# Optimization experiments

Hardware: AMD Instinct MI355X
Metric: run time of the kernel (lower is better)

Reference implementation:

```python
import jax, jax.numpy as jnp
import numpy as np
from jax import lax

CIN, COUT, K, PAD = 256, 128, 3, 1


def setup_inputs() -> dict:
    key = jax.random.key(0)
    ks = jax.random.split(key, 5)
    N, h0, w0 = 2, 64, 64
    x = jax.random.normal(ks[0], (N, CIN, h0, w0), jnp.float32)
    lateral_feat = jax.random.normal(ks[1], (N, COUT, 1, 1), jnp.float32)
    trans_w = jax.random.normal(ks[2], (CIN, COUT, K, K), jnp.float32) * 0.02
    off_w1 = jax.random.normal(ks[3], (64, COUT, 3, 3), jnp.float32) * 0.02
    off_b1 = jnp.zeros((64,), jnp.float32)
    off_w2 = jax.random.normal(ks[4], (2 * K * K, 64, 3, 3), jnp.float32) * 0.02
    off_b2 = jnp.zeros((2 * K * K,), jnp.float32)
    return dict(x=x, lateral_feat=lateral_feat, trans_w=trans_w,
                off_w1=off_w1, off_b1=off_b1, off_w2=off_w2, off_b2=off_b2)


def _conv2d(x, w, b, pad):
    y = lax.conv_general_dilated(x, w, (1, 1), [(pad, pad), (pad, pad)],
                                 dimension_numbers=('NCHW', 'OIHW', 'NCHW'))
    return y + b[None, :, None, None]


def _conv_transpose2d(x, w, stride, pad, out_pad):
    # torch ConvTranspose2d weight layout: [Cin, Cout, k, k]
    k = w.shape[2]
    wt = jnp.flip(w, (2, 3)).transpose(1, 0, 2, 3)  # [Cout, Cin, k, k]
    lo = k - 1 - pad
    hi = k - 1 - pad + out_pad
    return lax.conv_general_dilated(x, wt, (1, 1), [(lo, hi), (lo, hi)],
                                    lhs_dilation=(stride, stride),
                                    dimension_numbers=('NCHW', 'OIHW', 'NCHW'))


def _deform_conv2d(x, offset, w, pad):
    # x [N,C,H,W], offset [N,2*K*K,H,W] (y,x interleaved per kernel tap), w [O,C,K,K]
    N, C, H, W = x.shape
    O = w.shape[0]
    KK = K * K
    off = offset.reshape(N, KK, 2, H, W)
    ky = jnp.arange(KK) // K
    kx = jnp.arange(KK) % K
    py = jnp.arange(H)[None, None, :, None] + (ky - pad)[None, :, None, None] + off[:, :, 0]
    px = jnp.arange(W)[None, None, None, :] + (kx - pad)[None, :, None, None] + off[:, :, 1]
    y0 = jnp.floor(py)
    x0 = jnp.floor(px)
    dy = py - y0
    dx = px - x0
    y0i = y0.astype(jnp.int32)
    x0i = x0.astype(jnp.int32)
    xf = x.reshape(N, C, H * W)

    def corner(yi, xi, wgt):
        valid = (yi >= 0) & (yi < H) & (xi >= 0) & (xi < W)
        idx = (jnp.clip(yi, 0, H - 1) * W + jnp.clip(xi, 0, W - 1)).reshape(N, -1)
        v = jnp.take_along_axis(xf, idx[:, None, :], axis=2).reshape(N, C, KK, H, W)
        return v * (wgt * valid)[:, None]

    sampled = (corner(y0i, x0i, (1 - dy) * (1 - dx))
               + corner(y0i, x0i + 1, (1 - dy) * dx)
               + corner(y0i + 1, x0i, dy * (1 - dx))
               + corner(y0i + 1, x0i + 1, dy * dx))  # [N,C,KK,H,W]
    return jnp.einsum('nckhw,ock->nohw', sampled, w.reshape(O, C, KK))


def reference(x, lateral_feat, trans_w, off_w1, off_b1, off_w2, off_b2):
    up = _conv_transpose2d(x, trans_w, 2, PAD, 1)          # [N, COUT, 2h0, 2w0]
    h = jax.nn.relu(_conv2d(lateral_feat, off_w1, off_b1, 1))
    offset = jnp.tanh(_conv2d(h, off_w2, off_b2, 1))       # [N, 18, 1, 1]
    N, C, H, W = up.shape
    # offset.repeat(1, 1, H, W) with 1x1 spatial input == broadcast to full grid
    offset = jnp.broadcast_to(offset, (N, 2 * K * K, H, W))
    # deform_conv2d uses trans_conv weight [O=CIN, I=COUT, K, K], stride=1, pad=PAD
    return _deform_conv2d(up, offset, trans_w, PAD)        # [N, CIN, H, W]
```

## Files before the change

### kernel.cpp

```cpp
#include <hip/hip_runtime.h>
#include <hip/hip_fp16.h>
#include <math.h>

typedef __attribute__((ext_vector_type(8))) _Float16 f16x8;
typedef __attribute__((ext_vector_type(4))) float f32x4;

__device__ __forceinline__ unsigned short f2h(float f) {
    __half h = __float2half_rn(f);
    union { __half h; unsigned short u; } v; v.h = h; return v.u;
}
__device__ __forceinline__ unsigned pk2h(float lo, float hi) {
    __half2 h = __floats2half2_rn(lo, hi);
    union { __half2 h; unsigned u; } v; v.h = h; return v.u;
}

#define BARRIER() do { asm volatile("s_waitcnt lgkmcnt(0)" ::: "memory"); \
                       __builtin_amdgcn_s_barrier(); } while (0)

__device__ __forceinline__ void blend_store_h(uint4 uA, uint4 uB, uint4 uC, uint4 uD,
                                              __half2 w0, __half2 w1, __half2 w2, __half2 w3,
                                              unsigned short* dst) {
    union U { uint4 u; __half2 h[4]; };
    U a, b, c, d, r;
    a.u = uA; b.u = uB; c.u = uC; d.u = uD;
#pragma unroll
    for (int i = 0; i < 4; ++i)
        r.h[i] = __hfma2(w0, a.h[i], __hfma2(w1, b.h[i], __hfma2(w2, c.h[i], __hmul2(w3, d.h[i]))));
    *(uint4*)dst = r.u;
}

__global__ __launch_bounds__(256) void k_prep(const float* __restrict__ x,
                                              const float* __restrict__ lat,
                                              const float* __restrict__ tw,
                                              const float* __restrict__ w1,
                                              const float* __restrict__ b1,
                                              const float* __restrict__ w2,
                                              const float* __restrict__ b2,
                                              unsigned short* __restrict__ xp,
                                              unsigned short* __restrict__ A2f,
                                              unsigned short* __restrict__ Awf,
                                              unsigned short* __restrict__ upp,
                                              int* __restrict__ ipar,
                                              float* __restrict__ fpar) {
    __shared__ float sm[8420];
    int b = blockIdx.x, t = threadIdx.x;
    if (b == 0) {
        for (int i = t; i < 8192; i += 256) sm[(i >> 7) * 129 + (i & 127)] = w1[i * 9 + 4];
        __syncthreads();
        if (t < 128) {
            int n = t >> 6, o = t & 63;
            float s = b1[o];
            const float* ln = lat + n * 128;
#pragma unroll 8
            for (int c = 0; c < 128; ++c) s += ln[c] * sm[o * 129 + c];
            sm[8256 + t] = fmaxf(s, 0.f);
        }
        __syncthreads();
        if (t < 36) {
            int n = t / 18, j = t % 18;
            float s = b2[j];
            for (int o = 0; o < 64; ++o) s += sm[8256 + n * 64 + o] * w2[(j * 64 + o) * 9 + 4];
            float ov = tanhf(s);
            ov = fminf(fmaxf(ov, -0.999999f), 0.999999f);
            sm[8384 + t] = ov;
        }
        __syncthreads();
        if (t < 36) {
            int n = t / 18, j = t % 18;
            int tap = j >> 1, d = j & 1;
            float ov = sm[8384 + t];
            float fl = floorf(ov);
            int kc = d ? (tap % 3) : (tap / 3);
            ipar[(n * 9 + tap) * 2 + d] = kc - 1 + (int)fl;
            fpar[(n * 9 + tap) * 2 + d] = ov - fl;
        }
    } else if (b < 145) {
        int slot = (b - 1) * 256 + t;
        int l = slot & 63;
        int mi = (slot >> 6) & 3;
        int w = (slot >> 8) & 3;
        int k = slot >> 10;
        int row = w * 64 + mi * 16 + (l & 15);
        int kq = l >> 4;
        unsigned short v[8];
#pragma unroll
        for (int j = 0; j < 8; ++j) {
            int kcol = k * 32 + kq * 8 + j;
            int tap = kcol >> 7, c = kcol & 127;
            v[j] = f2h(tw[(row * 128 + c) * 9 + tap]);
        }
        unsigned p0 = (unsigned)v[0] | ((unsigned)v[1] << 16);
        unsigned p1 = (unsigned)v[2] | ((unsigned)v[3] << 16);
        unsigned p2 = (unsigned)v[4] | ((unsigned)v[5] << 16);
        unsigned p3 = (unsigned)v[6] | ((unsigned)v[7] << 16);
        *(uint4*)(A2f + slot * 8) = make_uint4(p0, p1, p2, p3);
    } else if (b < 289) {
        int slot = (b - 145) * 256 + t;
        int l = slot & 63;
        int mi = (slot >> 6) & 3;
        int wm = (slot >> 8) & 1;
        int k = slot >> 9;
        int row = wm * 64 + mi * 16 + (l & 15);
        int kq = l >> 4;
        unsigned short v[8];
#pragma unroll
        for (int j = 0; j < 8; ++j) {
            int kcol = k * 32 + kq * 8 + j;
            int t9 = kcol >> 8, ci = kcol & 255;
            int ky = t9 / 3, kx = t9 - ky * 3;
            v[j] = f2h(tw[(ci * 128 + row) * 9 + (2 - ky) * 3 + (2 - kx)]);
        }
        unsigned p0 = (unsigned)v[0] | ((unsigned)v[1] << 16);
        unsigned p1 = (unsigned)v[2] | ((unsigned)v[3] << 16);
        unsigned p2 = (unsigned)v[4] | ((unsigned)v[5] << 16);
        unsigned p3 = (unsigned)v[6] | ((unsigned)v[7] << 16);
        *(uint4*)(Awf + slot * 8) = make_uint4(p0, p1, p2, p3);
    } else if (b < 801) {
        int bb = b - 289;
        int h = bb & 63, cq = (bb >> 6) & 3, n = bb >> 8;
        int c0 = cq * 64;
        {
            int wcol = t & 63, sub = t >> 6;
            for (int r = 0; r < 16; ++r) {
                int ci_l = r * 4 + sub;
                sm[ci_l * 65 + wcol] = x[((n * 256 + c0 + ci_l) * 64 + h) * 64 + wcol];
            }
        }
        __syncthreads();
        int wcol = t >> 2, cg = t & 3;
        unsigned short* dst = xp + (size_t)n * (65 * 65 * 256) + (h * 65 + wcol) * 256 + c0 + cg * 16;
        unsigned pk[8];
#pragma unroll
        for (int j = 0; j < 8; ++j)
            pk[j] = pk2h(sm[(cg * 16 + 2 * j) * 65 + wcol], sm[(cg * 16 + 2 * j + 1) * 65 + wcol]);
        *(uint4*)dst = make_uint4(pk[0], pk[1], pk[2], pk[3]);
        *(uint4*)(dst + 8) = make_uint4(pk[4], pk[5], pk[6], pk[7]);
    } else if (b < 931) {
        int g = (b - 801) * 256 + t;
        int n2 = g >= 16640 ? 1 : 0;
        int i = g - n2 * 16640;
        int px_id = i >> 4, chv = i & 15;
        int r, c;
        if (px_id < 528) {
            int rr = px_id / 132;
            r = rr < 2 ? rr : 128 + rr;
            c = px_id - rr * 132;
        } else {
            int jj = px_id - 528;
            r = 2 + (jj >> 2);
            int cc = jj & 3;
            c = cc < 2 ? cc : 128 + cc;
        }
        uint4* p = (uint4*)(upp + (size_t)n2 * (132 * 132 * 128) + ((r * 132 + c) * 128) + chv * 8);
        *p = make_uint4(0u, 0u, 0u, 0u);
    } else {
        int g = (b - 931) * 256 + t;
        if (g < 8256) {
            int n2 = g >= 4128 ? 1 : 0;
            int i = g - n2 * 4128;
            int px_id = i >> 5, chv = i & 31;
            int h, wcol;
            if (px_id < 65) { h = 64; wcol = px_id; }
            else            { h = px_id - 65; wcol = 64; }
            uint4* p = (uint4*)(xp + (size_t)n2 * (65 * 65 * 256) + (h * 65 + wcol) * 256 + chv * 8);
            *p = make_uint4(0u, 0u, 0u, 0u);
        }
    }
}

__global__ __launch_bounds__(256) void k_tconv3(const unsigned short* __restrict__ xp,
                                                const unsigned short* __restrict__ Awf,
                                                unsigned short* __restrict__ upp) {
    __shared__ unsigned short Bs[2][2][64][40];
    __shared__ int st9[4];
    __shared__ int sbb[4];
    int t = threadIdx.x;
    int b = blockIdx.x;
    int phase = b & 1;
    int xpar = ((b >> 1) & 1) ^ phase;
    int n = (b >> 2) & 1;
    int yh = b >> 3;
    int y = yh * 2 + phase;
    const unsigned short* xpn = xp + (size_t)n * (65 * 65 * 256);

    int lane = t & 63, w = t >> 6;
    int col = lane & 15, q = lane >> 4;
    int wm = w >> 1, wn = w & 1;
    int bx = t >> 2, bcg = t & 3;
    int boff = bx * 256 + bcg * 8;

    int kys[2], kxs[2], nky, nkx;
    if (phase) { kys[0] = 0; kys[1] = 2; nky = 2; } else { kys[0] = 1; kys[1] = 1; nky = 1; }
    if (xpar)  { kxs[0] = 0; kxs[1] = 2; nkx = 2; } else { kxs[0] = 1; kxs[1] = 1; nkx = 1; }
    int nslots = nky * nkx;
    if (t < 4) {
        int tc = t < nslots ? t : 0;
        int a1 = (nkx == 2) ? (tc >> 1) : tc;
        int a2 = (nkx == 2) ? (tc & 1) : 0;
        int ky = kys[a1], kx = kxs[a2];
        st9[t] = ky * 3 + kx;
        int d2 = (y + ky - 1) >> 1;
        int s = (xpar + kx - 1) >> 1;
        sbb[t] = (d2 * 65 + s) * 256;
    }
    int NPAIR = nslots * 4;

    f32x4 acc[4][2];
#pragma unroll
    for (int mi = 0; mi < 4; ++mi)
#pragma unroll
        for (int ni = 0; ni < 2; ++ni) acc[mi][ni] = (f32x4){0.f, 0.f, 0.f, 0.f};

    __syncthreads();

    const unsigned short* Afw = Awf + wm * 2048 + lane * 8;
    f16x8 aC[2][4], aN[2][4];
    uint4 nb0, nb1;

    {
        const unsigned short* pT = xpn + sbb[0] + boff;
        uint4 b0 = *(const uint4*)pT;
        uint4 b1 = *(const uint4*)(pT + 32);
        const unsigned short* ap = Afw + st9[0] * 32768;
#pragma unroll
        for (int mi = 0; mi < 4; ++mi) {
            aC[0][mi] = *(const f16x8*)(ap + mi * 512);
            aC[1][mi] = *(const f16x8*)(ap + 4096 + mi * 512);
        }
        *(uint4*)&Bs[0][0][bx][bcg * 8] = b0;
        *(uint4*)&Bs[0][1][bx][bcg * 8] = b1;
    }
    BARRIER();

#define TC_PH(PP, BUF, AC, AN)                                                   \
    {                                                                            \
        int P_ = (PP);                                                           \
        if (P_ + 1 < NPAIR) {                                                    \
            int slot_ = (P_ + 1) >> 2;                                           \
            int cb0_ = ((P_ + 1) & 3) * 2;                                       \
            const unsigned short* pT_ = xpn + sbb[slot_] + cb0_ * 32 + boff;     \
            nb0 = *(const uint4*)pT_;                                            \
            nb1 = *(const uint4*)(pT_ + 32);                                     \
            const unsigned short* ap_ = Afw + (st9[slot_] * 8 + cb0_) * 4096;    \
            _Pragma("unroll")                                                    \
            for (int mi = 0; mi < 4; ++mi) {                                     \
                AN[0][mi] = *(const f16x8*)(ap_ + mi * 512);                     \
                AN[1][mi] = *(const f16x8*)(ap_ + 4096 + mi * 512);              \
            }                                                                    \
        }                                                                        \
        f16x8 bb[2][2];                                                          \
        _Pragma("unroll")                                                        \
        for (int c = 0; c < 2; ++c)                                              \
            _Pragma("unroll")                                                    \
            for (int ni = 0; ni < 2; ++ni)                                       \
                bb[c][ni] = *(const f16x8*)&Bs[BUF][c][wn * 32 + ni * 16 + col][q * 8]; \
        _Pragma("unroll")                                                        \
        for (int c = 0; c < 2; ++c)                                              \
            _Pragma("unroll")                                                    \
            for (int mi = 0; mi < 4; ++mi)                                       \
                _Pragma("unroll")                                                \
                for (int ni = 0; ni < 2; ++ni)                                   \
                    acc[mi][ni] = __builtin_amdgcn_mfma_f32_16x16x32_f16(AC[c][mi], bb[c][ni], acc[mi][ni], 0, 0, 0); \
        if (P_ + 1 < NPAIR) {                                                    \
            *(uint4*)&Bs[BUF ^ 1][0][bx][bcg * 8] = nb0;                         \
            *(uint4*)&Bs[BUF ^ 1][1][bx][bcg * 8] = nb1;                         \
        }                                                                        \
        BARRIER();                                                               \
    }

    for (int pp = 0; pp < NPAIR; pp += 2) {
        TC_PH(pp,     0, aC, aN);
        TC_PH(pp + 1, 1, aN, aC);
    }
#undef TC_PH

    unsigned short* uppn = upp + (size_t)n * (132 * 132 * 128);
#pragma unroll
    for (int mi = 0; mi < 4; ++mi)
#pragma unroll
        for (int ni = 0; ni < 2; ++ni) {
            int co = wm * 64 + mi * 16 + q * 4;
            int p64 = wn * 32 + ni * 16 + col;
            int xg = 2 * p64 + xpar;
            unsigned short* p = uppn + ((y + 2) * 132 + (xg + 2)) * 128 + co;
            unsigned lo = pk2h(acc[mi][ni][0], acc[mi][ni][1]);
            unsigned hi = pk2h(acc[mi][ni][2], acc[mi][ni][3]);
            *(uint2*)p = make_uint2(lo, hi);
        }
}

__global__ __launch_bounds__(256) void k_deform4(const unsigned short* __restrict__ upp,
                                                 const unsigned short* __restrict__ A2f,
                                                 const int* __restrict__ ipar,
                                                 const float* __restrict__ fpar,
                                                 float* __restrict__ out) {
    __shared__ unsigned short Ws[2][5][68][32];
    __shared__ unsigned short Bs[2][2][64][40];
    __shared__ int sR0[9], sDx[9];
    __shared__ __half2 swh[9][4];
    int t = threadIdx.x;
    int b = blockIdx.x;
    int xcd = b & 7, j = b >> 3;
    int n = xcd >> 2, band = xcd & 3;
    int y = band * 32 + (j & 31);
    int tx0 = (j >> 5) * 64;
    const unsigned short* uppn = upp + (size_t)n * (132 * 132 * 128);

    int lane = t & 63, w = t >> 6;
    int col = lane & 15, q = lane >> 4;
    int bx = t >> 2, bcg = t & 3;

    if (t < 9) {
        int iy = ipar[(n * 9 + t) * 2 + 0], ix = ipar[(n * 9 + t) * 2 + 1];
        float fy = fpar[(n * 9 + t) * 2 + 0], fx = fpar[(n * 9 + t) * 2 + 1];
        sR0[t] = iy + 2;
        sDx[t] = ix + 2;
        swh[t][0] = __float2half2_rn((1.f - fy) * (1.f - fx));
        swh[t][1] = __float2half2_rn((1.f - fy) * fx);
        swh[t][2] = __float2half2_rn(fy * (1.f - fx));
        swh[t][3] = __float2half2_rn(fy * fx);
    }

    f32x4 acc[4][4];
#pragma unroll
    for (int mi = 0; mi < 4; ++mi)
#pragma unroll
        for (int ni = 0; ni < 4; ++ni) acc[mi][ni] = (f32x4){0.f, 0.f, 0.f, 0.f};

    __syncthreads();

    const unsigned short* Afw = A2f + w * 2048 + lane * 8;
    f16x8 aC[2][4], aN[2][4];

#define BLEND_WS(CHUNK, TAP, DST)                                                \
    {                                                                            \
        int r0_ = sR0[TAP], dx_ = sDx[TAP];                                      \
        const unsigned short* pA_ = &Ws[CHUNK][0][0][0] + (r0_ * 68 + bx + dx_) * 32 + bcg * 8; \
        uint4 uA_ = *(const uint4*)pA_;                                          \
        uint4 uB_ = *(const uint4*)(pA_ + 32);                                   \
        uint4 uC_ = *(const uint4*)(pA_ + 68 * 32);                              \
        uint4 uD_ = *(const uint4*)(pA_ + 68 * 32 + 32);                         \
        blend_store_h(uA_, uB_, uC_, uD_, swh[TAP][0], swh[TAP][1],              \
                      swh[TAP][2], swh[TAP][3], DST);                            \
    }

#define DEF_TAU(TAU, BUF, AC, AN, S)                                             \
    {                                                                            \
        if ((TAU) < 8) {                                                         \
            const unsigned short* ap_ = Afw + (((TAU) + 1) * 4 + (S) * 2) * 8192;\
            _Pragma("unroll")                                                    \
            for (int mi = 0; mi < 4; ++mi) {                                     \
                AN[0][mi] = *(const f16x8*)(ap_ + mi * 512);                     \
                AN[1][mi] = *(const f16x8*)(ap_ + 8192 + mi * 512);              \
            }                                                                    \
        }                                                                        \
        f16x8 bb[2][4];                                                          \
        _Pragma("unroll")                                                        \
        for (int c = 0; c < 2; ++c)                                              \
            _Pragma("unroll")                                                    \
            for (int ni = 0; ni < 4; ++ni)                                       \
                bb[c][ni] = *(const f16x8*)&Bs[BUF][c][ni * 16 + col][q * 8];    \
        _Pragma("unroll")                                                        \
        for (int c = 0; c < 2; ++c)                                              \
            _Pragma("unroll")                                                    \
            for (int mi = 0; mi < 4; ++mi)                                       \
                _Pragma("unroll")                                                \
                for (int ni = 0; ni < 4; ++ni)                                   \
                    acc[mi][ni] = __builtin_amdgcn_mfma_f32_16x16x32_f16(AC[c][mi], bb[c][ni], acc[mi][ni], 0, 0, 0); \
        if ((TAU) < 8) {                                                         \
            BLEND_WS(0, (TAU) + 1, &Bs[BUF ^ 1][0][bx][bcg * 8]);                \
            BLEND_WS(1, (TAU) + 1, &Bs[BUF ^ 1][1][bx][bcg * 8]);                \
        }                                                                        \
        BARRIER();                                                               \
    }

    for (int s = 0; s < 2; ++s) {
        for (int i = t; i < 2720; i += 256) {
            int c2 = i / 1360;
            int rem2 = i - c2 * 1360;
            int row = rem2 / 272;
            int rem = rem2 - row * 272;
            int px = rem >> 2, cg4 = rem & 3;
            uint4 v = *(const uint4*)&uppn[(size_t)((y + row) * 132 + tx0 + px) * 128 + s * 64 + c2 * 32 + cg4 * 8];
            *(uint4*)(&Ws[c2][0][0][0] + (row * 68 + px) * 32 + cg4 * 8) = v;
        }
        BARRIER();
        {
            const unsigned short* ap0 = Afw + s * 16384;
#pragma unroll
            for (int mi = 0; mi < 4; ++mi) {
                aC[0][mi] = *(const f16x8*)(ap0 + mi * 512);
                aC[1][mi] = *(const f16x8*)(ap0 + 8192 + mi * 512);
            }
            BLEND_WS(0, 0, &Bs[0][0][bx][bcg * 8]);
            BLEND_WS(1, 0, &Bs[0][1][bx][bcg * 8]);
        }
        BARRIER();
        DEF_TAU(0, 0, aC, aN, s);
        DEF_TAU(1, 1, aN, aC, s);
        DEF_TAU(2, 0, aC, aN, s);
        DEF_TAU(3, 1, aN, aC, s);
        DEF_TAU(4, 0, aC, aN, s);
        DEF_TAU(5, 1, aN, aC, s);
        DEF_TAU(6, 0, aC, aN, s);
        DEF_TAU(7, 1, aN, aC, s);
        DEF_TAU(8, 0, aC, aN, s);
    }
#undef DEF_TAU
#undef BLEND_WS

#pragma unroll
    for (int mi = 0; mi < 4; ++mi)
#pragma unroll
        for (int ni = 0; ni < 4; ++ni) {
            int o = w * 64 + mi * 16 + q * 4;
            int xg = tx0 + ni * 16 + col;
            float* p = out + (((size_t)(n * 256 + o)) * 128 + y) * 128 + xg;
            p[0]         = acc[mi][ni][0];
            p[16384]     = acc[mi][ni][1];
            p[2 * 16384] = acc[mi][ni][2];
            p[3 * 16384] = acc[mi][ni][3];
        }
}

extern "C" void kernel_launch(void* const* d_in, const int* in_sizes, int n_in,
                              void* d_out, int out_size, void* d_ws, size_t ws_size,
                              hipStream_t stream) {
    const float* x   = (const float*)d_in[0];
    const float* lat = (const float*)d_in[1];
    const float* tw  = (const float*)d_in[2];
    const float* w1  = (const float*)d_in[3];
    const float* b1  = (const float*)d_in[4];
    const float* w2  = (const float*)d_in[5];
    const float* b2  = (const float*)d_in[6];
    float* out = (float*)d_out;

    char* ws = (char*)d_ws;
    unsigned short* upp = (unsigned short*)ws;
    unsigned short* xp  = (unsigned short*)(ws + 8921088);
    unsigned short* A2f = (unsigned short*)(ws + 13247488);
    unsigned short* Awf = (unsigned short*)(ws + 13837312);
    int*   ipar         = (int*)(ws + 14427136);
    float* fpar         = (float*)(ws + 14427424);

    k_prep<<<964, 256, 0, stream>>>(x, lat, tw, w1, b1, w2, b2, xp, A2f, Awf, upp, ipar, fpar);
    k_tconv3<<<512, 256, 0, stream>>>(xp, Awf, upp);
    k_deform4<<<512, 256, 0, stream>>>(upp, A2f, ipar, fpar, out);
}
```

Baseline: 129.6 us.

## Blend deform samples directly into MFMA B fragments, drop staging buffer and barriers

The deform kernel no longer writes bilinear-blended samples into a double-buffered shared Bs tile that is then re-read as MFMA operands. Each lane now blends its own B fragment straight from the shared window Ws, using an XOR swizzle on the channel group to reduce bank conflicts. This removes the per-tap barriers and the Bs writes and reads. The cost is that every wave (4 waves) redundantly performs the same blend for the same B fragments, roughly quadrupling blend ALU work and Ws reads, and the blend is no longer overlapped with the previous tap's MFMAs.

```diff
diff --git a/kernel.cpp b/kernel.cpp
--- a/kernel.cpp
+++ b/kernel.cpp
@@ -16,18 +16,6 @@
 
 #define BARRIER() do { asm volatile("s_waitcnt lgkmcnt(0)" ::: "memory"); \
                        __builtin_amdgcn_s_barrier(); } while (0)
-
-__device__ __forceinline__ void blend_store_h(uint4 uA, uint4 uB, uint4 uC, uint4 uD,
-                                              __half2 w0, __half2 w1, __half2 w2, __half2 w3,
-                                              unsigned short* dst) {
-    union U { uint4 u; __half2 h[4]; };
-    U a, b, c, d, r;
-    a.u = uA; b.u = uB; c.u = uC; d.u = uD;
-#pragma unroll
-    for (int i = 0; i < 4; ++i)
-        r.h[i] = __hfma2(w0, a.h[i], __hfma2(w1, b.h[i], __hfma2(w2, c.h[i], __hmul2(w3, d.h[i]))));
-    *(uint4*)dst = r.u;
-}
 
 __global__ __launch_bounds__(256) void k_prep(const float* __restrict__ x,
                                               const float* __restrict__ lat,
@@ -289,13 +277,12 @@
         }
 }
 
-__global__ __launch_bounds__(256) void k_deform4(const unsigned short* __restrict__ upp,
+__global__ __launch_bounds__(256) void k_deform5(const unsigned short* __restrict__ upp,
                                                  const unsigned short* __restrict__ A2f,
                                                  const int* __restrict__ ipar,
                                                  const float* __restrict__ fpar,
                                                  float* __restrict__ out) {
     __shared__ unsigned short Ws[2][5][68][32];
-    __shared__ unsigned short Bs[2][2][64][40];
     __shared__ int sR0[9], sDx[9];
     __shared__ __half2 swh[9][4];
     int t = threadIdx.x;
@@ -308,7 +295,6 @@
 
     int lane = t & 63, w = t >> 6;
     int col = lane & 15, q = lane >> 4;
-    int bx = t >> 2, bcg = t & 3;
 
     if (t < 9) {
         int iy = ipar[(n * 9 + t) * 2 + 0], ix = ipar[(n * 9 + t) * 2 + 1];
@@ -327,24 +313,33 @@
 #pragma unroll
         for (int ni = 0; ni < 4; ++ni) acc[mi][ni] = (f32x4){0.f, 0.f, 0.f, 0.f};
 
-    __syncthreads();
-
     const unsigned short* Afw = A2f + w * 2048 + lane * 8;
     f16x8 aC[2][4], aN[2][4];
 
-#define BLEND_WS(CHUNK, TAP, DST)                                                \
+    union BU { uint4 u; f16x8 v; __half2 h[4]; };
+
+#define BLEND_FRAG(C2, NI, TAP, OUTV)                                            \
     {                                                                            \
         int r0_ = sR0[TAP], dx_ = sDx[TAP];                                      \
-        const unsigned short* pA_ = &Ws[CHUNK][0][0][0] + (r0_ * 68 + bx + dx_) * 32 + bcg * 8; \
-        uint4 uA_ = *(const uint4*)pA_;                                          \
-        uint4 uB_ = *(const uint4*)(pA_ + 32);                                   \
-        uint4 uC_ = *(const uint4*)(pA_ + 68 * 32);                              \
-        uint4 uD_ = *(const uint4*)(pA_ + 68 * 32 + 32);                         \
-        blend_store_h(uA_, uB_, uC_, uD_, swh[TAP][0], swh[TAP][1],              \
-                      swh[TAP][2], swh[TAP][3], DST);                            \
-    }
-
-#define DEF_TAU(TAU, BUF, AC, AN, S)                                             \
+        int pe_ = (NI) * 16 + col + dx_;                                         \
+        const unsigned short* b0_ = &Ws[C2][0][0][0];                            \
+        const unsigned short* pA_ = b0_ + (r0_ * 68 + pe_) * 32 + ((q ^ ((pe_ >> 1) & 3)) * 8); \
+        const unsigned short* pB_ = b0_ + (r0_ * 68 + pe_ + 1) * 32 + ((q ^ (((pe_ + 1) >> 1) & 3)) * 8); \
+        BU au_, bu_, cu_, du_, ru_;                                              \
+        au_.u = *(const uint4*)pA_;                                              \
+        bu_.u = *(const uint4*)pB_;                                              \
+        cu_.u = *(const uint4*)(pA_ + 68 * 32);                                  \
+        du_.u = *(const uint4*)(pB_ + 68 * 32);                                  \
+        __half2 w0_ = swh[TAP][0], w1_ = swh[TAP][1];                            \
+        __half2 w2_ = swh[TAP][2], w3_ = swh[TAP][3];                            \
+        _Pragma("unroll")                                                        \
+        for (int i_ = 0; i_ < 4; ++i_)                                           \
+            ru_.h[i_] = __hfma2(w0_, au_.h[i_], __hfma2(w1_, bu_.h[i_],          \
+                        __hfma2(w2_, cu_.h[i_], __hmul2(w3_, du_.h[i_]))));      \
+        OUTV = ru_.v;                                                            \
+    }
+
+#define DEF_TAU5(TAU, AC, AN, S)                                                 \
     {                                                                            \
         if ((TAU) < 8) {                                                         \
             const unsigned short* ap_ = Afw + (((TAU) + 1) * 4 + (S) * 2) * 8192;\
@@ -359,7 +354,7 @@
         for (int c = 0; c < 2; ++c)                                              \
             _Pragma("unroll")                                                    \
             for (int ni = 0; ni < 4; ++ni)                                       \
-                bb[c][ni] = *(const f16x8*)&Bs[BUF][c][ni * 16 + col][q * 8];    \
+                BLEND_FRAG(c, ni, TAU, bb[c][ni]);                               \
         _Pragma("unroll")                                                        \
         for (int c = 0; c < 2; ++c)                                              \
             _Pragma("unroll")                                                    \
@@ -367,14 +362,10 @@
                 _Pragma("unroll")                                                \
                 for (int ni = 0; ni < 4; ++ni)                                   \
                     acc[mi][ni] = __builtin_amdgcn_mfma_f32_16x16x32_f16(AC[c][mi], bb[c][ni], acc[mi][ni], 0, 0, 0); \
-        if ((TAU) < 8) {                                                         \
-            BLEND_WS(0, (TAU) + 1, &Bs[BUF ^ 1][0][bx][bcg * 8]);                \
-            BLEND_WS(1, (TAU) + 1, &Bs[BUF ^ 1][1][bx][bcg * 8]);                \
-        }                                                                        \
-        BARRIER();                                                               \
     }
 
     for (int s = 0; s < 2; ++s) {
+        if (s) __syncthreads();
         for (int i = t; i < 2720; i += 256) {
             int c2 = i / 1360;
             int rem2 = i - c2 * 1360;
@@ -382,9 +373,9 @@
             int rem = rem2 - row * 272;
             int px = rem >> 2, cg4 = rem & 3;
             uint4 v = *(const uint4*)&uppn[(size_t)((y + row) * 132 + tx0 + px) * 128 + s * 64 + c2 * 32 + cg4 * 8];
-            *(uint4*)(&Ws[c2][0][0][0] + (row * 68 + px) * 32 + cg4 * 8) = v;
-        }
-        BARRIER();
+            *(uint4*)(&Ws[c2][0][0][0] + (row * 68 + px) * 32 + ((cg4 ^ ((px >> 1) & 3)) * 8)) = v;
+        }
+        __syncthreads();
         {
             const unsigned short* ap0 = Afw + s * 16384;
 #pragma unroll
@@ -392,22 +383,19 @@
                 aC[0][mi] = *(const f16x8*)(ap0 + mi * 512);
                 aC[1][mi] = *(const f16x8*)(ap0 + 8192 + mi * 512);
             }
-            BLEND_WS(0, 0, &Bs[0][0][bx][bcg * 8]);
-            BLEND_WS(1, 0, &Bs[0][1][bx][bcg * 8]);
-        }
-        BARRIER();
-        DEF_TAU(0, 0, aC, aN, s);
-        DEF_TAU(1, 1, aN, aC, s);
-        DEF_TAU(2, 0, aC, aN, s);
-        DEF_TAU(3, 1, aN, aC, s);
-        DEF_TAU(4, 0, aC, aN, s);
-        DEF_TAU(5, 1, aN, aC, s);
-        DEF_TAU(6, 0, aC, aN, s);
-        DEF_TAU(7, 1, aN, aC, s);
-        DEF_TAU(8, 0, aC, aN, s);
-    }
-#undef DEF_TAU
-#undef BLEND_WS
+        }
+        DEF_TAU5(0, aC, aN, s);
+        DEF_TAU5(1, aN, aC, s);
+        DEF_TAU5(2, aC, aN, s);
+        DEF_TAU5(3, aN, aC, s);
+        DEF_TAU5(4, aC, aN, s);
+        DEF_TAU5(5, aN, aC, s);
+        DEF_TAU5(6, aC, aN, s);
+        DEF_TAU5(7, aN, aC, s);
+        DEF_TAU5(8, aC, aN, s);
+    }
+#undef DEF_TAU5
+#undef BLEND_FRAG
 
 #pragma unroll
     for (int mi = 0; mi < 4; ++mi)
@@ -445,5 +433,5 @@
 
     k_prep<<<964, 256, 0, stream>>>(x, lat, tw, w1, b1, w2, b2, xp, A2f, Awf, upp, ipar, fpar);
     k_tconv3<<<512, 256, 0, stream>>>(xp, Awf, upp);
-    k_deform4<<<512, 256, 0, stream>>>(upp, A2f, ipar, fpar, out);
-}
+    k_deform5<<<512, 256, 0, stream>>>(upp, A2f, ipar, fpar, out);
+}
```

Result: slower. 135.0 us (+4.1%).
